# Optimization experiments

Hardware: AMD Instinct MI355X
Metric: run time of the kernel (lower is better)

The kernel has to match this reference:

```python
import jax, jax.numpy as jnp
import numpy as np

NF = 128  # latent_dim / number of filters


def setup_inputs() -> dict:
    key = jax.random.key(0)
    k1, k2, k3, k4 = jax.random.split(key, 4)
    B, H, W, C = 4, 64, 64, 128
    x = jax.random.normal(k1, (B, H, W, C), dtype=jnp.float32)
    y = jax.random.normal(k2, (B, H, W, C), dtype=jnp.float32)
    # 1x1 conv kernels (C_in, C_out) + biases, glorot-ish scale
    scale = 1.0 / np.sqrt(C)
    W1 = jax.random.normal(k3, (C, NF), dtype=jnp.float32) * scale
    W2 = jax.random.normal(k4, (C, NF), dtype=jnp.float32) * scale
    b1 = jnp.zeros((NF,), dtype=jnp.float32)
    b2 = jnp.zeros((NF,), dtype=jnp.float32)
    return {"x": x, "y": y, "W1": W1, "b1": b1, "W2": W2, "b2": b2}


def reference(x, y, W1, b1, W2, b2):
    B, H, Wd, C = x.shape
    hw = H * Wd
    # 1x1 convs == per-pixel matmul
    xq = jnp.einsum('bhwc,cf->bhwf', x, W1) + b1   # conv1(x)
    yk = jnp.einsum('bhwc,cf->bhwf', y, W2) + b2   # conv2(y)
    xq_r = xq.reshape(B, hw, NF)
    yk_r = yk.reshape(B, hw, NF)
    # A_ij = sigmoid(y_i . x_j), full (hw x hw) sigmoid attention
    A = jax.nn.sigmoid(jnp.einsum('bic,bjc->bij', yk_r, xq_r))
    out = jnp.einsum('bij,bjc->bic', A, yk_r).reshape(B, H, Wd, NF)
    # residual add of the *projected* x (matches original: x was overwritten by conv1)
    out = out + xq
    return out
```

## Files before the change

kernel.cpp:

```cpp
#include <hip/hip_runtime.h>
#include <hip/hip_bf16.h>
#include <stdint.h>

typedef float f32x16 __attribute__((ext_vector_type(16)));
typedef float f32x4  __attribute__((ext_vector_type(4)));
typedef short s16x8  __attribute__((ext_vector_type(8)));
typedef unsigned int u32x4 __attribute__((ext_vector_type(4)));

#define HWSZ   4096
#define NBATCH 4
#define LOG2E  1.44269504088896340736f

__device__ __forceinline__ unsigned short f2bf(float f) {
    unsigned u = __builtin_bit_cast(unsigned, f);
    u += 0x7FFFu + ((u >> 16) & 1u);
    return (unsigned short)(u >> 16);
}
__device__ __forceinline__ unsigned cvt_pk_bf16(float lo, float hi) {
    __hip_bfloat162 h = __float22bfloat162_rn(make_float2(lo, hi));
    return *reinterpret_cast<unsigned*>(&h);
}

__global__ __launch_bounds__(256, 1) void proj_kernel(
    const float* __restrict__ x, const float* __restrict__ y,
    const float* __restrict__ W1, const float* __restrict__ b1,
    const float* __restrict__ W2, const float* __restrict__ b2,
    float* __restrict__ xq_f32,
    unsigned short* __restrict__ xq_bf,
    unsigned short* __restrict__ yk_bf,
    unsigned short* __restrict__ ykT_bf)
{
    __shared__ unsigned short Xlds[64][136];
    __shared__ unsigned short Ylds[64][136];
    __shared__ unsigned short Tlds[128][72];

    const int t    = threadIdx.x;
    const int lane = t & 63;
    const int w    = t >> 6;
    const int l31  = lane & 31;
    const int g    = lane >> 5;
    const int r0   = blockIdx.x * 64;
    const int b    = r0 >> 12;
    const int j0   = r0 & (HWSZ - 1);

    #pragma unroll
    for (int i = 0; i < 8; ++i) {
        int li = t + 256 * i;
        int row = li >> 5, c = (li & 31) * 4;
        float4 vx = *(const float4*)(x + (size_t)(r0 + row) * 128 + c);
        float4 vy = *(const float4*)(y + (size_t)(r0 + row) * 128 + c);
        *(uint2*)&Xlds[row][c] = make_uint2(cvt_pk_bf16(vx.x, vx.y), cvt_pk_bf16(vx.z, vx.w));
        *(uint2*)&Ylds[row][c] = make_uint2(cvt_pk_bf16(vy.x, vy.y), cvt_pk_bf16(vy.z, vy.w));
    }
    __syncthreads();

    const int m  = w >> 1;
    const int fh = w & 1;
    const float* Wm = m ? W2 : W1;
    const float* bm = m ? b2 : b1;
    const unsigned short* A0 = m ? &Ylds[0][0] : &Xlds[0][0];

    f32x16 acc[2][2];
    #pragma unroll
    for (int i = 0; i < 16; ++i) {
        acc[0][0][i] = 0.f; acc[0][1][i] = 0.f;
        acc[1][0][i] = 0.f; acc[1][1][i] = 0.f;
    }

    #pragma unroll
    for (int ks = 0; ks < 8; ++ks) {
        s16x8 bfr[2];
        #pragma unroll
        for (int ft = 0; ft < 2; ++ft) {
            const float* wp = Wm + (size_t)(ks * 16 + g * 8) * 128 + fh * 64 + ft * 32 + l31;
            #pragma unroll
            for (int i = 0; i < 8; ++i)
                bfr[ft][i] = (short)f2bf(wp[(size_t)i * 128]);
        }
        #pragma unroll
        for (int rt = 0; rt < 2; ++rt) {
            s16x8 af = *(const s16x8*)(A0 + (size_t)(rt * 32 + l31) * 136 + ks * 16 + g * 8);
            acc[rt][0] = __builtin_amdgcn_mfma_f32_32x32x16_bf16(af, bfr[0], acc[rt][0], 0, 0, 0);
            acc[rt][1] = __builtin_amdgcn_mfma_f32_32x32x16_bf16(af, bfr[1], acc[rt][1], 0, 0, 0);
        }
    }

    const float bias_v[2] = { bm[fh * 64 + l31], bm[fh * 64 + 32 + l31] };

    if (m == 0) {
        #pragma unroll
        for (int rt = 0; rt < 2; ++rt)
        #pragma unroll
        for (int ft = 0; ft < 2; ++ft) {
            int f = fh * 64 + ft * 32 + l31;
            #pragma unroll
            for (int r = 0; r < 16; ++r) {
                int row = rt * 32 + (r & 3) + 8 * (r >> 2) + 4 * g;
                float v = acc[rt][ft][r] + bias_v[ft];
                size_t o = (size_t)(r0 + row) * 128 + f;
                xq_f32[o] = v;
                xq_bf[o]  = f2bf(v * LOG2E);
            }
        }
    } else {
        #pragma unroll
        for (int rt = 0; rt < 2; ++rt)
        #pragma unroll
        for (int ft = 0; ft < 2; ++ft) {
            int f = fh * 64 + ft * 32 + l31;
            #pragma unroll
            for (int rg = 0; rg < 4; ++rg) {
                float p0 = acc[rt][ft][4 * rg + 0] + bias_v[ft];
                float p1 = acc[rt][ft][4 * rg + 1] + bias_v[ft];
                float p2 = acc[rt][ft][4 * rg + 2] + bias_v[ft];
                float p3 = acc[rt][ft][4 * rg + 3] + bias_v[ft];
                int jb = rt * 32 + 8 * rg + 4 * g;
                *(uint2*)&Tlds[f][jb] = make_uint2(cvt_pk_bf16(p0, p1), cvt_pk_bf16(p2, p3));
                size_t o = (size_t)(r0 + jb) * 128 + f;
                yk_bf[o]       = f2bf(p0);
                yk_bf[o + 128] = f2bf(p1);
                yk_bf[o + 256] = f2bf(p2);
                yk_bf[o + 384] = f2bf(p3);
            }
        }
    }
    __syncthreads();

    {
        int f  = t >> 1;
        int jh = (t & 1) * 32;
        unsigned short* dst = ykT_bf + ((size_t)(b * 128 + f)) * HWSZ + j0 + jh;
        #pragma unroll
        for (int c = 0; c < 4; ++c)
            *(s16x8*)(dst + c * 8) = *(const s16x8*)&Tlds[f][jh + c * 8];
    }
}

#define KT_STR   136
#define VT_STR   72
#define KT_BYTES (64 * KT_STR * 2)
#define VT_BYTES (128 * VT_STR * 2)
#define BUF_BYTES (KT_BYTES + VT_BYTES)

__global__ __launch_bounds__(256, 2) void attn128_kernel(
    const unsigned short* __restrict__ Kbf,
    const unsigned short* __restrict__ Qbf,
    const unsigned short* __restrict__ Vtbf,
    float* __restrict__ outp)
{
    __shared__ __align__(16) char smem[2 * BUF_BYTES];

    const int t    = threadIdx.x;
    const int lane = t & 63;
    const int qt   = t >> 6;
    const int l31  = lane & 31;
    const int g    = lane >> 5;

    const int split  = blockIdx.x >> 7;
    const int r      = blockIdx.x & 127;
    const int b      = r >> 5;
    const int qb     = (r & 31) * 128;
    const int jBegin = split * (HWSZ / 4);
    const int nt     = (HWSZ / 4) / 64;

    s16x8 qfrag[8];
    {
        const unsigned short* qp =
            Qbf + (((size_t)(b * HWSZ + qb + 32 * qt + l31)) << 7) + g * 8;
        #pragma unroll
        for (int fs = 0; fs < 8; ++fs)
            qfrag[fs] = *(const s16x8*)(qp + fs * 16);
    }

    f32x16 acc[4];
    #pragma unroll
    for (int ft = 0; ft < 4; ++ft)
        #pragma unroll
        for (int i = 0; i < 16; ++i) acc[ft][i] = 0.f;

    const unsigned short* Kbase = Kbf  + (((size_t)b * HWSZ) << 7);
    const unsigned short* Vbase = Vtbf + (((size_t)b) << 7) * HWSZ;

    const unsigned short* kSrc = Kbase + (size_t)(jBegin + (t >> 4)) * 128 + (t & 15) * 8;
    const unsigned short* vSrc = Vbase + (size_t)(t >> 3) * HWSZ + jBegin + (t & 7) * 8;
    const int kDst = (t >> 4) * KT_STR + (t & 15) * 8;
    const int vDst = (t >> 3) * VT_STR + (t & 7) * 8;

    {
        unsigned short* Kl = (unsigned short*)smem;
        unsigned short* Vl = (unsigned short*)(smem + KT_BYTES);
        #pragma unroll
        for (int i = 0; i < 4; ++i)
            *(s16x8*)(Kl + kDst + i * 16 * KT_STR) = *(const s16x8*)(kSrc + (size_t)i * 2048);
        #pragma unroll
        for (int i = 0; i < 4; ++i)
            *(s16x8*)(Vl + vDst + i * 32 * VT_STR) = *(const s16x8*)(vSrc + (size_t)i * 32 * HWSZ);
    }
    __syncthreads();

    int c = 0;
    for (int it = 0; it < nt; ++it) {
        const bool pre = (it + 1 < nt);
        const unsigned short* Kl = (const unsigned short*)(smem + c * BUF_BYTES);
        const unsigned short* Vl = (const unsigned short*)(smem + c * BUF_BYTES + KT_BYTES);

        s16x8 kf[16];
        #pragma unroll
        for (int jt = 0; jt < 2; ++jt) {
            const unsigned short* Krow = Kl + (size_t)(32 * jt + l31) * KT_STR + g * 8;
            #pragma unroll
            for (int fs = 0; fs < 8; ++fs)
                kf[jt * 8 + fs] = *(const s16x8*)(Krow + fs * 16);
        }

        f32x16 s0a, s0b, s1a, s1b;
        #pragma unroll
        for (int i = 0; i < 16; ++i) { s0a[i] = 0.f; s0b[i] = 0.f; s1a[i] = 0.f; s1b[i] = 0.f; }
        __builtin_amdgcn_s_setprio(1);
        #pragma unroll
        for (int fs = 0; fs < 4; ++fs) {
            s0a = __builtin_amdgcn_mfma_f32_32x32x16_bf16(kf[fs],         qfrag[fs],     s0a, 0, 0, 0);
            s0b = __builtin_amdgcn_mfma_f32_32x32x16_bf16(kf[fs + 4],     qfrag[fs + 4], s0b, 0, 0, 0);
            s1a = __builtin_amdgcn_mfma_f32_32x32x16_bf16(kf[8 + fs],     qfrag[fs],     s1a, 0, 0, 0);
            s1b = __builtin_amdgcn_mfma_f32_32x32x16_bf16(kf[8 + fs + 4], qfrag[fs + 4], s1b, 0, 0, 0);
        }
        __builtin_amdgcn_s_setprio(0);

        s16x8 kr[4], vr[4];
        if (pre) {
            kSrc += 64 * 128;
            vSrc += 64;
            #pragma unroll
            for (int i = 0; i < 4; ++i)
                kr[i] = *(const s16x8*)(kSrc + (size_t)i * 2048);
            #pragma unroll
            for (int i = 0; i < 4; ++i)
                vr[i] = *(const s16x8*)(vSrc + (size_t)i * 32 * HWSZ);
        }

        unsigned W0[2][4], W1[2][4];
        {
            f32x16 sv0, sv1;
            #pragma unroll
            for (int i = 0; i < 16; ++i) { sv0[i] = s0a[i] + s0b[i]; sv1[i] = s1a[i] + s1b[i]; }
            #pragma unroll
            for (int rg = 0; rg < 4; ++rg) {
                float a0 = __builtin_amdgcn_rcpf(1.f + __builtin_amdgcn_exp2f(-sv0[4 * rg + 0]));
                float a1 = __builtin_amdgcn_rcpf(1.f + __builtin_amdgcn_exp2f(-sv0[4 * rg + 1]));
                float a2 = __builtin_amdgcn_rcpf(1.f + __builtin_amdgcn_exp2f(-sv0[4 * rg + 2]));
                float a3 = __builtin_amdgcn_rcpf(1.f + __builtin_amdgcn_exp2f(-sv0[4 * rg + 3]));
                float b0 = __builtin_amdgcn_rcpf(1.f + __builtin_amdgcn_exp2f(-sv1[4 * rg + 0]));
                float b1 = __builtin_amdgcn_rcpf(1.f + __builtin_amdgcn_exp2f(-sv1[4 * rg + 1]));
                float b2 = __builtin_amdgcn_rcpf(1.f + __builtin_amdgcn_exp2f(-sv1[4 * rg + 2]));
                float b3 = __builtin_amdgcn_rcpf(1.f + __builtin_amdgcn_exp2f(-sv1[4 * rg + 3]));
                W0[0][rg] = cvt_pk_bf16(a0, a1);
                W1[0][rg] = cvt_pk_bf16(a2, a3);
                W0[1][rg] = cvt_pk_bf16(b0, b1);
                W1[1][rg] = cvt_pk_bf16(b2, b3);
            }
        }

        __builtin_amdgcn_s_setprio(1);
        #pragma unroll
        for (int jt = 0; jt < 2; ++jt)
        #pragma unroll
        for (int s2 = 0; s2 < 2; ++s2) {
            unsigned a0 = W0[jt][2 * s2], b0 = W0[jt][2 * s2 + 1];
            unsigned a1 = W1[jt][2 * s2], b1 = W1[jt][2 * s2 + 1];
            asm("v_permlane32_swap_b32 %0, %1" : "+v"(a0), "+v"(b0));
            asm("v_permlane32_swap_b32 %0, %1" : "+v"(a1), "+v"(b1));
            u32x4 pw;
            pw[0] = a0; pw[1] = a1; pw[2] = b0; pw[3] = b1;
            s16x8 pf = __builtin_bit_cast(s16x8, pw);
            const int ks = 2 * jt + s2;
            #pragma unroll
            for (int ft = 0; ft < 4; ++ft) {
                s16x8 vf = *(const s16x8*)(Vl + (size_t)(32 * ft + l31) * VT_STR + ks * 16 + g * 8);
                acc[ft] = __builtin_amdgcn_mfma_f32_32x32x16_bf16(pf, vf, acc[ft], 0, 0, 0);
            }
        }
        __builtin_amdgcn_s_setprio(0);

        if (pre) {
            unsigned short* Kd = (unsigned short*)(smem + (c ^ 1) * BUF_BYTES);
            unsigned short* Vd = (unsigned short*)(smem + (c ^ 1) * BUF_BYTES + KT_BYTES);
            #pragma unroll
            for (int i = 0; i < 4; ++i)
                *(s16x8*)(Kd + kDst + i * 16 * KT_STR) = kr[i];
            #pragma unroll
            for (int i = 0; i < 4; ++i)
                *(s16x8*)(Vd + vDst + i * 32 * VT_STR) = vr[i];
        }
        __syncthreads();
        c ^= 1;
    }

    float* op = outp + (size_t)split * ((size_t)NBATCH * HWSZ * 128);
    #pragma unroll
    for (int ft = 0; ft < 4; ++ft)
    #pragma unroll
    for (int r2 = 0; r2 < 16; ++r2) {
        int row = (r2 & 3) + 8 * (r2 >> 2) + 4 * g;
        int q = qb + 32 * qt + row;
        size_t o = (((size_t)(b * HWSZ + q)) << 7) + 32 * ft + l31;
        op[o] = acc[ft][r2];
    }
}

template<bool SPLIT>
__global__ __launch_bounds__(256, 2) void attn_kernel(
    const unsigned short* __restrict__ Kbf,
    const unsigned short* __restrict__ Qbf,
    const unsigned short* __restrict__ Vtbf,
    const float* __restrict__ resid,
    float* __restrict__ outp)
{
    __shared__ __align__(16) char smem[2 * BUF_BYTES];

    const int t    = threadIdx.x;
    const int lane = t & 63;
    const int w    = t >> 6;
    const int qt   = w & 1;
    const int jt   = w >> 1;
    const int l31  = lane & 31;
    const int g    = lane >> 5;

    int bid = blockIdx.x;
    int half = 0;
    if (SPLIT) { half = bid >> 8; bid &= 255; }
    const int b      = bid >> 6;
    const int qb     = (bid & 63) * 64;
    const int jBegin = half * (HWSZ / 2);
    const int nt     = (SPLIT ? HWSZ / 2 : HWSZ) / 64;

    s16x8 qfrag[8];
    {
        const unsigned short* qp =
            Qbf + (((size_t)(b * HWSZ + qb + 32 * qt + l31)) << 7) + g * 8;
        #pragma unroll
        for (int fs = 0; fs < 8; ++fs)
            qfrag[fs] = *(const s16x8*)(qp + fs * 16);
    }

    f32x16 acc[4];
    #pragma unroll
    for (int ft = 0; ft < 4; ++ft)
        #pragma unroll
        for (int i = 0; i < 16; ++i) acc[ft][i] = 0.f;

    const unsigned short* Kbase = Kbf  + (((size_t)b * HWSZ) << 7);
    const unsigned short* Vbase = Vtbf + (((size_t)b) << 7) * HWSZ;

    const unsigned short* kSrc = Kbase + (size_t)(jBegin + (t >> 4)) * 128 + (t & 15) * 8;
    const unsigned short* vSrc = Vbase + (size_t)(t >> 3) * HWSZ + jBegin + (t & 7) * 8;
    const int kDst = (t >> 4) * KT_STR + (t & 15) * 8;
    const int vDst = (t >> 3) * VT_STR + (t & 7) * 8;

    {
        unsigned short* Kl = (unsigned short*)smem;
        unsigned short* Vl = (unsigned short*)(smem + KT_BYTES);
        #pragma unroll
        for (int i = 0; i < 4; ++i)
            *(s16x8*)(Kl + kDst + i * 16 * KT_STR) = *(const s16x8*)(kSrc + (size_t)i * 2048);
        #pragma unroll
        for (int i = 0; i < 4; ++i)
            *(s16x8*)(Vl + vDst + i * 32 * VT_STR) = *(const s16x8*)(vSrc + (size_t)i * 32 * HWSZ);
    }
    __syncthreads();

    int c = 0;
    for (int it = 0; it < nt; ++it) {
        const bool pre = (it + 1 < nt);
        s16x8 kr[4], vr[4];
        if (pre) {
            kSrc += 64 * 128;
            vSrc += 64;
            #pragma unroll
            for (int i = 0; i < 4; ++i)
                kr[i] = *(const s16x8*)(kSrc + (size_t)i * 2048);
            #pragma unroll
            for (int i = 0; i < 4; ++i)
                vr[i] = *(const s16x8*)(vSrc + (size_t)i * 32 * HWSZ);
        }

        const unsigned short* Kl = (const unsigned short*)(smem + c * BUF_BYTES);
        const unsigned short* Vl = (const unsigned short*)(smem + c * BUF_BYTES + KT_BYTES);

        f32x16 sa, sb;
        #pragma unroll
        for (int i = 0; i < 16; ++i) { sa[i] = 0.f; sb[i] = 0.f; }
        const unsigned short* Krow = Kl + (size_t)(32 * jt + l31) * KT_STR + g * 8;
        __builtin_amdgcn_s_setprio(1);
        #pragma unroll
        for (int fs = 0; fs < 4; ++fs) {
            sa = __builtin_amdgcn_mfma_f32_32x32x16_bf16(
                     *(const s16x8*)(Krow + fs * 16), qfrag[fs], sa, 0, 0, 0);
            sb = __builtin_amdgcn_mfma_f32_32x32x16_bf16(
                     *(const s16x8*)(Krow + (fs + 4) * 16), qfrag[fs + 4], sb, 0, 0, 0);
        }
        __builtin_amdgcn_s_setprio(0);

        unsigned W0[4], W1[4];
        #pragma unroll
        for (int rg = 0; rg < 4; ++rg) {
            float s0 = sa[4 * rg + 0] + sb[4 * rg + 0];
            float s1 = sa[4 * rg + 1] + sb[4 * rg + 1];
            float s2v = sa[4 * rg + 2] + sb[4 * rg + 2];
            float s3 = sa[4 * rg + 3] + sb[4 * rg + 3];
            float p0 = __builtin_amdgcn_rcpf(1.f + __builtin_amdgcn_exp2f(-s0));
            float p1 = __builtin_amdgcn_rcpf(1.f + __builtin_amdgcn_exp2f(-s1));
            float p2 = __builtin_amdgcn_rcpf(1.f + __builtin_amdgcn_exp2f(-s2v));
            float p3 = __builtin_amdgcn_rcpf(1.f + __builtin_amdgcn_exp2f(-s3));
            W0[rg] = cvt_pk_bf16(p0, p1);
            W1[rg] = cvt_pk_bf16(p2, p3);
        }

        #pragma unroll
        for (int s2 = 0; s2 < 2; ++s2) {
            unsigned a0 = W0[2 * s2], b0 = W0[2 * s2 + 1];
            unsigned a1 = W1[2 * s2], b1 = W1[2 * s2 + 1];
            asm("v_permlane32_swap_b32 %0, %1" : "+v"(a0), "+v"(b0));
            asm("v_permlane32_swap_b32 %0, %1" : "+v"(a1), "+v"(b1));
            u32x4 pw;
            pw[0] = a0; pw[1] = a1; pw[2] = b0; pw[3] = b1;
            s16x8 pf = __builtin_bit_cast(s16x8, pw);
            const int ks = 2 * jt + s2;
            __builtin_amdgcn_s_setprio(1);
            #pragma unroll
            for (int ft = 0; ft < 4; ++ft) {
                s16x8 vf = *(const s16x8*)(Vl + (size_t)(32 * ft + l31) * VT_STR + ks * 16 + g * 8);
                acc[ft] = __builtin_amdgcn_mfma_f32_32x32x16_bf16(pf, vf, acc[ft], 0, 0, 0);
            }
            __builtin_amdgcn_s_setprio(0);
        }

        if (pre) {
            unsigned short* Kd = (unsigned short*)(smem + (c ^ 1) * BUF_BYTES);
            unsigned short* Vd = (unsigned short*)(smem + (c ^ 1) * BUF_BYTES + KT_BYTES);
            #pragma unroll
            for (int i = 0; i < 4; ++i)
                *(s16x8*)(Kd + kDst + i * 16 * KT_STR) = kr[i];
            #pragma unroll
            for (int i = 0; i < 4; ++i)
                *(s16x8*)(Vd + vDst + i * 32 * VT_STR) = vr[i];
        }
        __syncthreads();
        c ^= 1;
    }

    float* red = (float*)smem;
    if (jt == 1) {
        #pragma unroll
        for (int ft = 0; ft < 4; ++ft)
        #pragma unroll
        for (int r = 0; r < 16; ++r) {
            int row = (r & 3) + 8 * (r >> 2) + 4 * g;
            red[qt * 4096 + row * 128 + 32 * ft + l31] = acc[ft][r];
        }
    }
    __syncthreads();
    if (jt == 0) {
        float* op = outp + (SPLIT ? (size_t)half * ((size_t)NBATCH * HWSZ * 128) : 0);
        #pragma unroll
        for (int ft = 0; ft < 4; ++ft)
        #pragma unroll
        for (int r = 0; r < 16; ++r) {
            int row = (r & 3) + 8 * (r >> 2) + 4 * g;
            float v = acc[ft][r] + red[qt * 4096 + row * 128 + 32 * ft + l31];
            int q = qb + 32 * qt + row;
            size_t o = (((size_t)(b * HWSZ + q)) << 7) + 32 * ft + l31;
            if (SPLIT) op[o] = v;
            else       op[o] = v + resid[o];
        }
    }
}

__global__ __launch_bounds__(256, 1) void reduce2_kernel(
    const float* __restrict__ p0, const float* __restrict__ p1, float* outp)
{
    int i = blockIdx.x * 256 + threadIdx.x;
    f32x4 a = ((const f32x4*)p0)[i];
    f32x4 b = ((const f32x4*)p1)[i];
    f32x4 c = ((f32x4*)outp)[i];
    ((f32x4*)outp)[i] = a + b + c;
}

template<int S>
__global__ __launch_bounds__(256, 1) void reduceN_kernel(
    const float* __restrict__ parts, float* __restrict__ outp)
{
    const size_t N4 = (size_t)NBATCH * HWSZ * 128 / 4;
    size_t i = (size_t)blockIdx.x * 256 + threadIdx.x;
    f32x4 s = ((f32x4*)outp)[i];
    #pragma unroll
    for (int k = 0; k < S; ++k)
        s += ((const f32x4*)parts)[i + (size_t)k * N4];
    ((f32x4*)outp)[i] = s;
}

extern "C" void kernel_launch(void* const* d_in, const int* in_sizes, int n_in,
                              void* d_out, int out_size, void* d_ws, size_t ws_size,
                              hipStream_t stream) {
    const float* x  = (const float*)d_in[0];
    const float* y  = (const float*)d_in[1];
    const float* W1 = (const float*)d_in[2];
    const float* b1 = (const float*)d_in[3];
    const float* W2 = (const float*)d_in[4];
    const float* b2 = (const float*)d_in[5];
    float* out = (float*)d_out;

    const size_t NELEM = (size_t)NBATCH * HWSZ * 128;
    unsigned short* xq_bf  = (unsigned short*)d_ws;
    unsigned short* yk_bf  = xq_bf + NELEM;
    unsigned short* ykT_bf = yk_bf + NELEM;
    float* part = (float*)(ykT_bf + NELEM);

    proj_kernel<<<(int)(NBATCH * HWSZ / 64), 256, 0, stream>>>(
        x, y, W1, b1, W2, b2, out, xq_bf, yk_bf, ykT_bf);

    if (ws_size >= NELEM * (6 + 16)) {
        attn128_kernel<<<512, 256, 0, stream>>>(xq_bf, yk_bf, ykT_bf, part);
        reduceN_kernel<4><<<(int)(NELEM / 1024), 256, 0, stream>>>(part, out);
    } else if (ws_size >= NELEM * (6 + 8)) {
        attn_kernel<true><<<512, 256, 0, stream>>>(xq_bf, yk_bf, ykT_bf, out, part);
        reduce2_kernel<<<(int)(NELEM / 1024), 256, 0, stream>>>(part, part + NELEM, out);
    } else {
        attn_kernel<false><<<256, 256, 0, stream>>>(xq_bf, yk_bf, ykT_bf, out, out);
    }
}
```

Before: 67.76 us.

## Software-pipeline QK MFMAs with sigmoid and PV MFMAs across key halves

Splits the per-tile score computation into two 32-key halves and interleaves them. The second half's QK MFMAs are issued alongside the first half's sigmoid, and the second half's sigmoid runs between the first half's PV MFMAs. The K fragment loads for the second half are also deferred. The goal is to overlap transcendental VALU work with matrix-core work instead of running them in separate phases, which could shift register pressure and scheduling.

Result: faster. 65.84 us (-2.8%).

```diff
diff --git a/kernel.cpp b/kernel.cpp
--- a/kernel.cpp
+++ b/kernel.cpp
@@ -19,6 +19,9 @@
 __device__ __forceinline__ unsigned cvt_pk_bf16(float lo, float hi) {
     __hip_bfloat162 h = __float22bfloat162_rn(make_float2(lo, hi));
     return *reinterpret_cast<unsigned*>(&h);
+}
+__device__ __forceinline__ float sigm2(float s) {
+    return __builtin_amdgcn_rcpf(1.f + __builtin_amdgcn_exp2f(-s));
 }
 
 __global__ __launch_bounds__(256, 1) void proj_kernel(
@@ -204,28 +207,30 @@
         const unsigned short* Kl = (const unsigned short*)(smem + c * BUF_BYTES);
         const unsigned short* Vl = (const unsigned short*)(smem + c * BUF_BYTES + KT_BYTES);
 
-        s16x8 kf[16];
-        #pragma unroll
-        for (int jt = 0; jt < 2; ++jt) {
-            const unsigned short* Krow = Kl + (size_t)(32 * jt + l31) * KT_STR + g * 8;
+        s16x8 kf0[8], kf1[8];
+        {
+            const unsigned short* Krow = Kl + (size_t)l31 * KT_STR + g * 8;
             #pragma unroll
             for (int fs = 0; fs < 8; ++fs)
-                kf[jt * 8 + fs] = *(const s16x8*)(Krow + fs * 16);
-        }
-
-        f32x16 s0a, s0b, s1a, s1b;
-        #pragma unroll
-        for (int i = 0; i < 16; ++i) { s0a[i] = 0.f; s0b[i] = 0.f; s1a[i] = 0.f; s1b[i] = 0.f; }
+                kf0[fs] = *(const s16x8*)(Krow + fs * 16);
+        }
+        f32x16 s0a, s0b;
+        #pragma unroll
+        for (int i = 0; i < 16; ++i) { s0a[i] = 0.f; s0b[i] = 0.f; }
         __builtin_amdgcn_s_setprio(1);
         #pragma unroll
         for (int fs = 0; fs < 4; ++fs) {
-            s0a = __builtin_amdgcn_mfma_f32_32x32x16_bf16(kf[fs],         qfrag[fs],     s0a, 0, 0, 0);
-            s0b = __builtin_amdgcn_mfma_f32_32x32x16_bf16(kf[fs + 4],     qfrag[fs + 4], s0b, 0, 0, 0);
-            s1a = __builtin_amdgcn_mfma_f32_32x32x16_bf16(kf[8 + fs],     qfrag[fs],     s1a, 0, 0, 0);
-            s1b = __builtin_amdgcn_mfma_f32_32x32x16_bf16(kf[8 + fs + 4], qfrag[fs + 4], s1b, 0, 0, 0);
+            s0a = __builtin_amdgcn_mfma_f32_32x32x16_bf16(kf0[fs],     qfrag[fs],     s0a, 0, 0, 0);
+            s0b = __builtin_amdgcn_mfma_f32_32x32x16_bf16(kf0[fs + 4], qfrag[fs + 4], s0b, 0, 0, 0);
         }
         __builtin_amdgcn_s_setprio(0);
 
+        {
+            const unsigned short* Krow = Kl + (size_t)(32 + l31) * KT_STR + g * 8;
+            #pragma unroll
+            for (int fs = 0; fs < 8; ++fs)
+                kf1[fs] = *(const s16x8*)(Krow + fs * 16);
+        }
         s16x8 kr[4], vr[4];
         if (pre) {
             kSrc += 64 * 128;
@@ -238,41 +243,60 @@
                 vr[i] = *(const s16x8*)(vSrc + (size_t)i * 32 * HWSZ);
         }
 
+        f32x16 s1a, s1b;
+        #pragma unroll
+        for (int i = 0; i < 16; ++i) { s1a[i] = 0.f; s1b[i] = 0.f; }
         unsigned W0[2][4], W1[2][4];
-        {
-            f32x16 sv0, sv1;
-            #pragma unroll
-            for (int i = 0; i < 16; ++i) { sv0[i] = s0a[i] + s0b[i]; sv1[i] = s1a[i] + s1b[i]; }
-            #pragma unroll
-            for (int rg = 0; rg < 4; ++rg) {
-                float a0 = __builtin_amdgcn_rcpf(1.f + __builtin_amdgcn_exp2f(-sv0[4 * rg + 0]));
-                float a1 = __builtin_amdgcn_rcpf(1.f + __builtin_amdgcn_exp2f(-sv0[4 * rg + 1]));
-                float a2 = __builtin_amdgcn_rcpf(1.f + __builtin_amdgcn_exp2f(-sv0[4 * rg + 2]));
-                float a3 = __builtin_amdgcn_rcpf(1.f + __builtin_amdgcn_exp2f(-sv0[4 * rg + 3]));
-                float b0 = __builtin_amdgcn_rcpf(1.f + __builtin_amdgcn_exp2f(-sv1[4 * rg + 0]));
-                float b1 = __builtin_amdgcn_rcpf(1.f + __builtin_amdgcn_exp2f(-sv1[4 * rg + 1]));
-                float b2 = __builtin_amdgcn_rcpf(1.f + __builtin_amdgcn_exp2f(-sv1[4 * rg + 2]));
-                float b3 = __builtin_amdgcn_rcpf(1.f + __builtin_amdgcn_exp2f(-sv1[4 * rg + 3]));
-                W0[0][rg] = cvt_pk_bf16(a0, a1);
-                W1[0][rg] = cvt_pk_bf16(a2, a3);
-                W0[1][rg] = cvt_pk_bf16(b0, b1);
-                W1[1][rg] = cvt_pk_bf16(b2, b3);
-            }
+        #pragma unroll
+        for (int fs = 0; fs < 4; ++fs) {
+            s1a = __builtin_amdgcn_mfma_f32_32x32x16_bf16(kf1[fs],     qfrag[fs],     s1a, 0, 0, 0);
+            s1b = __builtin_amdgcn_mfma_f32_32x32x16_bf16(kf1[fs + 4], qfrag[fs + 4], s1b, 0, 0, 0);
+            const int rg = fs;
+            float p0 = sigm2(s0a[4 * rg + 0] + s0b[4 * rg + 0]);
+            float p1 = sigm2(s0a[4 * rg + 1] + s0b[4 * rg + 1]);
+            float p2 = sigm2(s0a[4 * rg + 2] + s0b[4 * rg + 2]);
+            float p3 = sigm2(s0a[4 * rg + 3] + s0b[4 * rg + 3]);
+            W0[0][rg] = cvt_pk_bf16(p0, p1);
+            W1[0][rg] = cvt_pk_bf16(p2, p3);
         }
 
         __builtin_amdgcn_s_setprio(1);
         #pragma unroll
-        for (int jt = 0; jt < 2; ++jt)
-        #pragma unroll
         for (int s2 = 0; s2 < 2; ++s2) {
-            unsigned a0 = W0[jt][2 * s2], b0 = W0[jt][2 * s2 + 1];
-            unsigned a1 = W1[jt][2 * s2], b1 = W1[jt][2 * s2 + 1];
+            unsigned a0 = W0[0][2 * s2], b0 = W0[0][2 * s2 + 1];
+            unsigned a1 = W1[0][2 * s2], b1 = W1[0][2 * s2 + 1];
             asm("v_permlane32_swap_b32 %0, %1" : "+v"(a0), "+v"(b0));
             asm("v_permlane32_swap_b32 %0, %1" : "+v"(a1), "+v"(b1));
             u32x4 pw;
             pw[0] = a0; pw[1] = a1; pw[2] = b0; pw[3] = b1;
             s16x8 pf = __builtin_bit_cast(s16x8, pw);
-            const int ks = 2 * jt + s2;
+            #pragma unroll
+            for (int ft = 0; ft < 4; ++ft) {
+                s16x8 vf = *(const s16x8*)(Vl + (size_t)(32 * ft + l31) * VT_STR + s2 * 16 + g * 8);
+                acc[ft] = __builtin_amdgcn_mfma_f32_32x32x16_bf16(pf, vf, acc[ft], 0, 0, 0);
+            }
+            #pragma unroll
+            for (int h = 0; h < 2; ++h) {
+                const int rg = 2 * s2 + h;
+                float p0 = sigm2(s1a[4 * rg + 0] + s1b[4 * rg + 0]);
+                float p1 = sigm2(s1a[4 * rg + 1] + s1b[4 * rg + 1]);
+                float p2 = sigm2(s1a[4 * rg + 2] + s1b[4 * rg + 2]);
+                float p3 = sigm2(s1a[4 * rg + 3] + s1b[4 * rg + 3]);
+                W0[1][rg] = cvt_pk_bf16(p0, p1);
+                W1[1][rg] = cvt_pk_bf16(p2, p3);
+            }
+        }
+
+        #pragma unroll
+        for (int s2 = 0; s2 < 2; ++s2) {
+            unsigned a0 = W0[1][2 * s2], b0 = W0[1][2 * s2 + 1];
+            unsigned a1 = W1[1][2 * s2], b1 = W1[1][2 * s2 + 1];
+            asm("v_permlane32_swap_b32 %0, %1" : "+v"(a0), "+v"(b0));
+            asm("v_permlane32_swap_b32 %0, %1" : "+v"(a1), "+v"(b1));
+            u32x4 pw;
+            pw[0] = a0; pw[1] = a1; pw[2] = b0; pw[3] = b1;
+            s16x8 pf = __builtin_bit_cast(s16x8, pw);
+            const int ks = 2 + s2;
             #pragma unroll
             for (int ft = 0; ft < 4; ++ft) {
                 s16x8 vf = *(const s16x8*)(Vl + (size_t)(32 * ft + l31) * VT_STR + ks * 16 + g * 8);
@@ -403,14 +427,10 @@
         unsigned W0[4], W1[4];
         #pragma unroll
         for (int rg = 0; rg < 4; ++rg) {
-            float s0 = sa[4 * rg + 0] + sb[4 * rg + 0];
-            float s1 = sa[4 * rg + 1] + sb[4 * rg + 1];
-            float s2v = sa[4 * rg + 2] + sb[4 * rg + 2];
-            float s3 = sa[4 * rg + 3] + sb[4 * rg + 3];
-            float p0 = __builtin_amdgcn_rcpf(1.f + __builtin_amdgcn_exp2f(-s0));
-            float p1 = __builtin_amdgcn_rcpf(1.f + __builtin_amdgcn_exp2f(-s1));
-            float p2 = __builtin_amdgcn_rcpf(1.f + __builtin_amdgcn_exp2f(-s2v));
-            float p3 = __builtin_amdgcn_rcpf(1.f + __builtin_amdgcn_exp2f(-s3));
+            float p0 = sigm2(sa[4 * rg + 0] + sb[4 * rg + 0]);
+            float p1 = sigm2(sa[4 * rg + 1] + sb[4 * rg + 1]);
+            float p2 = sigm2(sa[4 * rg + 2] + sb[4 * rg + 2]);
+            float p3 = sigm2(sa[4 * rg + 3] + sb[4 * rg + 3]);
             W0[rg] = cvt_pk_bf16(p0, p1);
             W1[rg] = cvt_pk_bf16(p2, p3);
         }
```
